# Optimization experiments

Measured on AMD Instinct MI355X. Metric: run time of the kernel, lower is better.

## Reference

```python
import jax, jax.numpy as jnp
import numpy as np

BS, N, DX, DE, DY, NH = 4, 256, 256, 64, 64, 8
DF = DX // NH


def setup_inputs() -> dict:
    key = jax.random.key(0)
    ks = jax.random.split(key, 24)

    def w(k, i, o):
        return jax.random.normal(k, (i, o), jnp.float32) / jnp.sqrt(jnp.float32(i))

    d = {}
    d["x"] = jax.random.normal(ks[0], (BS, N, DX), jnp.float32)
    d["e"] = jax.random.normal(ks[1], (BS, N, N, DE), jnp.float32)
    d["y"] = jax.random.normal(ks[2], (BS, DY), jnp.float32)
    d["node_mask"] = jnp.ones((BS, N), jnp.float32)
    # projections (use_bias=False in the module)
    d["Wq"] = w(ks[3], DX, DX)
    d["Wk"] = w(ks[4], DX, DX)
    d["Wv"] = w(ks[5], DX, DX)
    d["We_mul"] = w(ks[6], DE, DX)
    d["We_add"] = w(ks[7], DE, DX)
    d["Wye_add"] = w(ks[8], DY, DX)
    d["Wye_mul"] = w(ks[9], DY, DX)
    d["Wyx_add"] = w(ks[10], DY, DX)
    d["Wyx_mul"] = w(ks[11], DY, DX)
    d["Wyy"] = w(ks[12], DY, DY)
    # pooled-feature -> y maps (Xtoy / Etoy use 4*d features: mean,min,max,std)
    d["Wxy"] = w(ks[13], 4 * DX, DY)
    d["bxy"] = jnp.zeros((DY,), jnp.float32)
    d["Wey"] = w(ks[14], 4 * DE, DY)
    d["bey"] = jnp.zeros((DY,), jnp.float32)
    # output heads (bias=True, flax Dense default)
    d["We_out"] = w(ks[15], DX, DE)
    d["be_out"] = jnp.zeros((DE,), jnp.float32)
    d["Wx_out"] = w(ks[16], DX, DX)
    d["bx_out"] = jnp.zeros((DX,), jnp.float32)
    d["Wy_out"] = w(ks[17], DY, DY)
    d["by_out"] = jnp.zeros((DY,), jnp.float32)
    return d


def reference(x, e, y, node_mask, Wq, Wk, Wv, We_mul, We_add, Wye_add, Wye_mul,
              Wyx_add, Wyx_mul, Wyy, Wxy, bxy, Wey, bey, We_out, be_out,
              Wx_out, bx_out, Wy_out, by_out):
    bs, n, dx = x.shape
    nh, df = NH, DF
    x_mask = node_mask[..., None]                       # (bs,n,1)
    e_mask1 = x_mask[:, :, None, :]                     # (bs,n,1,1)
    e_mask2 = x_mask[:, None, :, :]                     # (bs,1,n,1)
    em = e_mask1 * e_mask2                              # (bs,n,n,1)

    q = (x @ Wq) * x_mask
    k = (x @ Wk) * x_mask
    Q = q.reshape(bs, n, 1, nh, df)                     # (bs,n,1,h,df)
    K = k.reshape(bs, 1, n, nh, df)                     # (bs,1,n,h,df)
    Y = Q * K / jnp.sqrt(jnp.float32(df))               # (bs,n,n,h,df) per-channel scores

    e1 = ((e @ We_mul) * em).reshape(bs, n, n, nh, df)
    e2 = ((e @ We_add) * em).reshape(bs, n, n, nh, df)
    Y = Y * (e1 + 1.0) + e2                             # FiLM by edges

    newE = Y.reshape(bs, n, n, dx)
    ye1 = (y @ Wye_add)[:, None, None, :]
    ye2 = (y @ Wye_mul)[:, None, None, :]
    newE = ye1 + (ye2 + 1.0) * newE                     # FiLM by global y
    newE = (newE @ We_out + be_out) * em                # (bs,n,n,de)

    # masked softmax over key axis (axis=2); mask broadcasts over df
    mask5 = e_mask2[..., None] > 0                      # (bs,1,n,1,1)
    attn = jax.nn.softmax(jnp.where(mask5, Y, -1e9), axis=2)

    v = ((x @ Wv) * x_mask).reshape(bs, 1, n, nh, df)
    weighted = (attn * v).sum(axis=2).reshape(bs, n, dx)

    yx1 = (y @ Wyx_add)[:, None, :]
    yx2 = (y @ Wyx_mul)[:, None, :]
    newX = yx1 + (yx2 + 1.0) * weighted
    newX = (newX @ Wx_out + bx_out) * x_mask            # (bs,n,dx)

    def pool(t, axes):
        return jnp.concatenate([t.mean(axis=axes), t.min(axis=axes),
                                t.max(axis=axes), t.std(axis=axes, ddof=1)], axis=-1)

    x_y = pool(x, (1,)) @ Wxy + bxy                     # (bs,dy)
    e_y = pool(e, (1, 2)) @ Wey + bey                   # (bs,dy)
    y_y = y @ Wyy
    newY = (y_y + e_y + x_y) @ Wy_out + by_out          # (bs,dy)
    return newX, newE, newY
```

## Files before the change

### kernel.cpp

```cpp
#include <hip/hip_runtime.h>
#include <hip/hip_bf16.h>

#define BSZ 4
#define NN  256
#define DXX 256
#define DEE 64
#define DYY 64

#define OFF_Q     0
#define OFF_K     262144
#define OFF_V     524288
#define OFF_XW    786432
#define OFF_YE1   1048576
#define OFF_YE2   1049600
#define OFF_YX1   1050624
#define OFF_YX2   1051648
#define OFF_PX    1052672
#define OFF_EPART 1057792

typedef __attribute__((ext_vector_type(8))) short bf16x8;
typedef __attribute__((ext_vector_type(4))) float f32x4;

__device__ __forceinline__ short f2bf(float f) {
    unsigned u = __float_as_uint(f);
    unsigned r = u + 0x7fffu + ((u >> 16) & 1u);
    return (short)(r >> 16);
}

__device__ __forceinline__ unsigned cvt_pk_bf16(float lo, float hi) {
    unsigned r;
    asm("v_cvt_pk_bf16_f32 %0, %1, %2" : "=v"(r) : "v"(lo), "v"(hi));
    return r;
}

__device__ __forceinline__ void pack8_store(const float4& A, const float4& B, short* dst) {
    uint4 v;
    v.x = cvt_pk_bf16(A.x, A.y);
    v.y = cvt_pk_bf16(A.z, A.w);
    v.z = cvt_pk_bf16(B.x, B.y);
    v.w = cvt_pk_bf16(B.z, B.w);
    *(uint4*)dst = v;
}

__global__ __launch_bounds__(256) void prep_kernel(
    const float* __restrict__ x, const float* __restrict__ e, const float* __restrict__ y,
    const float* __restrict__ nm,
    const float* __restrict__ Wq, const float* __restrict__ Wk, const float* __restrict__ Wv,
    const float* __restrict__ Wye_add, const float* __restrict__ Wye_mul,
    const float* __restrict__ Wyx_add, const float* __restrict__ Wyx_mul,
    float* __restrict__ ws) {

    __shared__ float smem[16 * 256];
    const int blk = blockIdx.x;
    const int t = threadIdx.x;

    if (blk < 192) {
        const int m0 = (blk & 63) * 16;
        const int which = blk >> 6;
        const float* W = which == 0 ? Wq : (which == 1 ? Wk : Wv);
        float* out = ws + (size_t)which * 262144;
        float (*xl)[256] = (float(*)[256])smem;
        for (int r = 0; r < 16; ++r) xl[r][t] = x[(m0 + r) * 256 + t];
        __syncthreads();
        float acc[16];
#pragma unroll
        for (int r = 0; r < 16; ++r) acc[r] = 0.f;
        for (int d = 0; d < 256; d += 4) {
            float w0 = W[(d + 0) * 256 + t];
            float w1 = W[(d + 1) * 256 + t];
            float w2 = W[(d + 2) * 256 + t];
            float w3 = W[(d + 3) * 256 + t];
#pragma unroll
            for (int r = 0; r < 16; ++r) {
                float4 ev = *(const float4*)&xl[r][d];
                acc[r] = fmaf(ev.x, w0, fmaf(ev.y, w1, fmaf(ev.z, w2, fmaf(ev.w, w3, acc[r]))));
            }
        }
#pragma unroll
        for (int r = 0; r < 16; ++r) {
            int m = m0 + r;
            out[m * 256 + t] = acc[r] * nm[m];
        }
    } else if (blk < 196) {
        const int b = blk - 192;
        float a1 = 0.f, a2 = 0.f, a3 = 0.f, a4 = 0.f;
        for (int k = 0; k < DYY; ++k) {
            float yv = y[b * DYY + k];
            a1 = fmaf(yv, Wye_add[k * 256 + t], a1);
            a2 = fmaf(yv, Wye_mul[k * 256 + t], a2);
            a3 = fmaf(yv, Wyx_add[k * 256 + t], a3);
            a4 = fmaf(yv, Wyx_mul[k * 256 + t], a4);
        }
        ws[OFF_YE1 + b * 256 + t] = a1;
        ws[OFF_YE2 + b * 256 + t] = a2;
        ws[OFF_YX1 + b * 256 + t] = a3;
        ws[OFF_YX2 + b * 256 + t] = a4;
    } else if (blk < 452) {
        const int idx = blk - 196;
        const int s = idx & 63, bb = idx >> 6;
        const int dq = (t & 15) * 4, g = t >> 4;
        const float* base = e + ((size_t)bb * 65536 + s * 1024) * 64;
        float s0 = 0.f, s1 = 0.f, s2 = 0.f, s3 = 0.f;
        float q0 = 0.f, q1 = 0.f, q2 = 0.f, q3 = 0.f;
        float mn0 = 1e30f, mn1 = 1e30f, mn2 = 1e30f, mn3 = 1e30f;
        float mx0 = -1e30f, mx1 = -1e30f, mx2 = -1e30f, mx3 = -1e30f;
#pragma unroll 4
        for (int rr = 0; rr < 64; ++rr) {
            const int row = g * 64 + rr;
            float4 v = *(const float4*)&base[row * 64 + dq];
            s0 += v.x; s1 += v.y; s2 += v.z; s3 += v.w;
            q0 = fmaf(v.x, v.x, q0); q1 = fmaf(v.y, v.y, q1);
            q2 = fmaf(v.z, v.z, q2); q3 = fmaf(v.w, v.w, q3);
            mn0 = fminf(mn0, v.x); mn1 = fminf(mn1, v.y);
            mn2 = fminf(mn2, v.z); mn3 = fminf(mn3, v.w);
            mx0 = fmaxf(mx0, v.x); mx1 = fmaxf(mx1, v.y);
            mx2 = fmaxf(mx2, v.z); mx3 = fmaxf(mx3, v.w);
        }
        float (*red)[16][64] = (float(*)[16][64])smem;
        red[0][g][dq + 0] = s0;  red[0][g][dq + 1] = s1;  red[0][g][dq + 2] = s2;  red[0][g][dq + 3] = s3;
        red[1][g][dq + 0] = q0;  red[1][g][dq + 1] = q1;  red[1][g][dq + 2] = q2;  red[1][g][dq + 3] = q3;
        red[2][g][dq + 0] = mn0; red[2][g][dq + 1] = mn1; red[2][g][dq + 2] = mn2; red[2][g][dq + 3] = mn3;
        red[3][g][dq + 0] = mx0; red[3][g][dq + 1] = mx1; red[3][g][dq + 2] = mx2; red[3][g][dq + 3] = mx3;
        __syncthreads();
        const int stat = t >> 6, d = t & 63;
        float a;
        if (stat < 2) {
            a = 0.f;
            for (int gg = 0; gg < 16; ++gg) a += red[stat][gg][d];
        } else if (stat == 2) {
            a = 1e30f;
            for (int gg = 0; gg < 16; ++gg) a = fminf(a, red[2][gg][d]);
        } else {
            a = -1e30f;
            for (int gg = 0; gg < 16; ++gg) a = fmaxf(a, red[3][gg][d]);
        }
        ws[OFF_EPART + (size_t)((bb * 64 + s) * 64 + d) * 4 + stat] = a;
    } else {
        const int b = blk - 452;
        float s = 0.f, q = 0.f, mn = 1e30f, mx = -1e30f;
        for (int i = 0; i < 256; ++i) {
            float v = x[(b * 256 + i) * 256 + t];
            s += v; q = fmaf(v, v, q);
            mn = fminf(mn, v); mx = fmaxf(mx, v);
        }
        float mean = s * (1.f / 256.f);
        float var  = (q - s * s * (1.f / 256.f)) * (1.f / 255.f);
        var = fmaxf(var, 0.f);
        ws[OFF_PX + b * 1024 + t]       = mean;
        ws[OFF_PX + b * 1024 + 256 + t] = mn;
        ws[OFF_PX + b * 1024 + 512 + t] = mx;
        ws[OFF_PX + b * 1024 + 768 + t] = sqrtf(var);
    }
}

#define EBP  72
#define YPLP 264
#define OBP  68

__global__ __launch_bounds__(256, 2) void fusedmfma_kernel(
    const float* __restrict__ e, const float* __restrict__ nmask,
    const float* __restrict__ Wm, const float* __restrict__ Wa,
    const float* __restrict__ We_out, const float* __restrict__ be_out,
    const float* __restrict__ ws, float* __restrict__ outE, float* __restrict__ xw) {

    const int i = blockIdx.x, b = blockIdx.y;
    const int tid  = threadIdx.x;
    const int w    = tid >> 6;
    const int lane = tid & 63;
    const int quad = lane >> 4, l16 = lane & 15;

    __shared__ __align__(16) short ebuf[2][32 * EBP];
    __shared__ __align__(16) short ypl[2][32 * YPLP];
    __shared__ __align__(16) float obuf[2][32 * OBP];
    __shared__ float nml[256];

    nml[tid] = nmask[b * 256 + tid];

    bf16x8 bm[4][2], ba[4][2], bw[8];
    const int cw = w * 64;
#pragma unroll
    for (int ct = 0; ct < 4; ++ct) {
        const int c = cw + ct * 16 + l16;
#pragma unroll
        for (int s = 0; s < 2; ++s) {
            bf16x8 t1, t2;
#pragma unroll
            for (int jj = 0; jj < 8; ++jj) {
                const int d = s * 32 + quad * 8 + jj;
                t1[jj] = f2bf(Wm[d * 256 + c]);
                t2[jj] = f2bf(Wa[d * 256 + c]);
            }
            bm[ct][s] = t1; ba[ct][s] = t2;
        }
    }
    const int cp = w * 16 + l16;
    {
#pragma unroll
        for (int s = 0; s < 8; ++s) {
            bf16x8 t;
#pragma unroll
            for (int jj = 0; jj < 8; ++jj) {
                const int cch = s * 32 + quad * 8 + jj;
                t[jj] = f2bf(We_out[cch * 64 + cp]);
            }
            bw[s] = t;
        }
    }
    const float bo = be_out[cp];

    const float rs = 0.17677669529663687f;
    float qc[4], ye1c[4], ye2c[4];
#pragma unroll
    for (int ct = 0; ct < 4; ++ct) {
        const int c = cw + ct * 16 + l16;
        qc[ct]   = ws[OFF_Q + (size_t)(b * 256 + i) * 256 + c] * rs;
        ye1c[ct] = ws[OFF_YE1 + b * 256 + c];
        ye2c[ct] = ws[OFF_YE2 + b * 256 + c] + 1.f;
    }
    const float* kb = ws + OFF_K + (size_t)b * 65536;
    const float* vb = ws + OFF_V + (size_t)b * 65536;

    const float* eb = e + ((size_t)(b * 256 + i)) * 256 * 64;
    const int jr = tid >> 3, c0 = (tid & 7) * 8;
    {
        float4 A = *(const float4*)(eb + jr * 64 + c0);
        float4 B = *(const float4*)(eb + jr * 64 + c0 + 4);
        pack8_store(A, B, &ebuf[0][jr * EBP + c0]);
    }
    __syncthreads();
    const float mi = nml[i];
    const size_t outbase = (size_t)(b * 256 + i) * 256;

    float msm[4], lsm[4], wsm[4];
#pragma unroll
    for (int ct = 0; ct < 4; ++ct) { msm[ct] = -1e30f; lsm[ct] = 0.f; wsm[ct] = 0.f; }

    for (int chunk = 0; chunk < 8; ++chunk) {
        const int cur = chunk & 1, j0 = chunk * 32;

        bf16x8 ae[2][2];
#pragma unroll
        for (int jt = 0; jt < 2; ++jt)
#pragma unroll
            for (int s = 0; s < 2; ++s)
                ae[jt][s] = *(const bf16x8*)&ebuf[cur][(jt * 16 + l16) * EBP + s * 32 + quad * 8];

        float4 pfA, pfB;
        if (chunk < 7) {
            const float* nb = eb + (size_t)(j0 + 32 + jr) * 64 + c0;
            pfA = *(const float4*)(nb);
            pfB = *(const float4*)(nb + 4);
        }

        float emv[8];
#pragma unroll
        for (int jt = 0; jt < 2; ++jt)
#pragma unroll
            for (int r = 0; r < 4; ++r)
                emv[jt * 4 + r] = mi * nml[j0 + jt * 16 + quad * 4 + r];

        for (int ct = 0; ct < 4; ++ct) {
            const int c = cw + ct * 16 + l16;
            float Ks[8], Vs[8];
#pragma unroll
            for (int jt = 0; jt < 2; ++jt)
#pragma unroll
                for (int r = 0; r < 4; ++r) {
                    const int jg = j0 + jt * 16 + quad * 4 + r;
                    Ks[jt * 4 + r] = kb[jg * 256 + c];
                    Vs[jt * 4 + r] = vb[jg * 256 + c];
                }

            f32x4 a1_0 = {0.f, 0.f, 0.f, 0.f}, a1_1 = {0.f, 0.f, 0.f, 0.f};
            f32x4 a2_0 = {0.f, 0.f, 0.f, 0.f}, a2_1 = {0.f, 0.f, 0.f, 0.f};
#pragma unroll
            for (int s = 0; s < 2; ++s) {
                a1_0 = __builtin_amdgcn_mfma_f32_16x16x32_bf16(ae[0][s], bm[ct][s], a1_0, 0, 0, 0);
                a1_1 = __builtin_amdgcn_mfma_f32_16x16x32_bf16(ae[1][s], bm[ct][s], a1_1, 0, 0, 0);
                a2_0 = __builtin_amdgcn_mfma_f32_16x16x32_bf16(ae[0][s], ba[ct][s], a2_0, 0, 0, 0);
                a2_1 = __builtin_amdgcn_mfma_f32_16x16x32_bf16(ae[1][s], ba[ct][s], a2_1, 0, 0, 0);
            }

            float Ys[8];
#pragma unroll
            for (int jt = 0; jt < 2; ++jt) {
                float yv[4];
#pragma unroll
                for (int r = 0; r < 4; ++r) {
                    const int u  = jt * 4 + r;
                    const float e1v = (jt == 0) ? a1_0[r] : a1_1[r];
                    const float e2v = (jt == 0) ? a2_0[r] : a2_1[r];
                    const float em = emv[u];
                    const float Yv = fmaf(qc[ct] * Ks[u], fmaf(e1v, em, 1.f), e2v * em);
                    yv[r] = fmaf(ye2c[ct], Yv, ye1c[ct]);
                    Ys[u] = (em > 0.f) ? Yv : -1e9f;
                }
                const int jl0 = jt * 16 + quad * 4;
                unsigned short* yb = (unsigned short*)&ypl[cur][jl0 * YPLP + c];
                const unsigned p01 = cvt_pk_bf16(yv[0], yv[1]);
                const unsigned p23 = cvt_pk_bf16(yv[2], yv[3]);
                yb[0]        = (unsigned short)p01;
                yb[YPLP]     = (unsigned short)(p01 >> 16);
                yb[2 * YPLP] = (unsigned short)p23;
                yb[3 * YPLP] = (unsigned short)(p23 >> 16);
            }
            float cm = Ys[0];
#pragma unroll
            for (int u = 1; u < 8; ++u) cm = fmaxf(cm, Ys[u]);
            const float mnew = fmaxf(msm[ct], cm);
            const float al = __expf(msm[ct] - mnew);
            float sum = 0.f, wsum = 0.f;
#pragma unroll
            for (int u = 0; u < 8; ++u) {
                const float p = __expf(Ys[u] - mnew);
                sum += p; wsum = fmaf(p, Vs[u], wsum);
            }
            lsm[ct] = fmaf(lsm[ct], al, sum);
            wsm[ct] = fmaf(wsm[ct], al, wsum);
            msm[ct] = mnew;
        }

        if (chunk < 7) pack8_store(pfA, pfB, &ebuf[cur ^ 1][jr * EBP + c0]);
        __syncthreads();

        f32x4 acc0 = {0.f, 0.f, 0.f, 0.f}, acc1 = {0.f, 0.f, 0.f, 0.f};
#pragma unroll
        for (int s = 0; s < 8; ++s) {
            bf16x8 a0 = *(const bf16x8*)&ypl[cur][(l16) * YPLP + s * 32 + quad * 8];
            bf16x8 a1 = *(const bf16x8*)&ypl[cur][(16 + l16) * YPLP + s * 32 + quad * 8];
            acc0 = __builtin_amdgcn_mfma_f32_16x16x32_bf16(a0, bw[s], acc0, 0, 0, 0);
            acc1 = __builtin_amdgcn_mfma_f32_16x16x32_bf16(a1, bw[s], acc1, 0, 0, 0);
        }
#pragma unroll
        for (int jt = 0; jt < 2; ++jt)
#pragma unroll
            for (int r = 0; r < 4; ++r) {
                const int jl = jt * 16 + quad * 4 + r;
                const float em2 = mi * nml[j0 + jl];
                const float av = (jt == 0) ? acc0[r] : acc1[r];
                obuf[cur][jl * OBP + cp] = (av + bo) * em2;
            }
        if (chunk > 0) {
            const int pj0 = j0 - 32;
            const float4 A  = *(const float4*)&obuf[cur ^ 1][jr * OBP + c0];
            const float4 Bv = *(const float4*)&obuf[cur ^ 1][jr * OBP + c0 + 4];
            float* dst = outE + (outbase + pj0 + jr) * 64 + c0;
            *(float4*)dst = A; *(float4*)(dst + 4) = Bv;
        }
    }
    __syncthreads();
    {
        const float4 A  = *(const float4*)&obuf[1][jr * OBP + c0];
        const float4 Bv = *(const float4*)&obuf[1][jr * OBP + c0 + 4];
        float* dst = outE + (outbase + 224 + jr) * 64 + c0;
        *(float4*)dst = A; *(float4*)(dst + 4) = Bv;
    }

#pragma unroll
    for (int ct = 0; ct < 4; ++ct) {
        float m = msm[ct], l = lsm[ct], wv = wsm[ct];
#pragma unroll
        for (int off = 16; off < 64; off <<= 1) {
            const float m2 = __shfl_xor(m, off, 64);
            const float l2 = __shfl_xor(l, off, 64);
            const float w2 = __shfl_xor(wv, off, 64);
            const float mn = fmaxf(m, m2);
            const float s1 = __expf(m - mn), s2 = __expf(m2 - mn);
            l = l * s1 + l2 * s2;
            wv = wv * s1 + w2 * s2;
            m = mn;
        }
        if (quad == 0) {
            const int c = cw + ct * 16 + l16;
            const float weighted = wv / l;
            const float yx1 = ws[OFF_YX1 + b * 256 + c];
            const float yx2 = ws[OFF_YX2 + b * 256 + c] + 1.f;
            xw[(size_t)(b * 256 + i) * 256 + c] = fmaf(yx2, weighted, yx1);
        }
    }
}

__global__ __launch_bounds__(256) void post_kernel(
    const float* __restrict__ xwin, const float* __restrict__ Wx_out,
    const float* __restrict__ bx_out, const float* __restrict__ nm,
    const float* __restrict__ y,
    const float* __restrict__ Wyy, const float* __restrict__ Wxy,
    const float* __restrict__ bxy, const float* __restrict__ Wey,
    const float* __restrict__ bey, const float* __restrict__ Wy_out,
    const float* __restrict__ by_out,
    const float* __restrict__ ws, float* __restrict__ outX, float* __restrict__ outY) {

    __shared__ float smem[16 * 256];
    const int blk = blockIdx.x;
    const int t = threadIdx.x;

    if (blk < 64) {
        const int m0 = blk * 16;
        float (*xl)[256] = (float(*)[256])smem;
        for (int r = 0; r < 16; ++r) xl[r][t] = xwin[(m0 + r) * 256 + t];
        __syncthreads();
        float acc[16];
#pragma unroll
        for (int r = 0; r < 16; ++r) acc[r] = 0.f;
        for (int d = 0; d < 256; d += 4) {
            float w0 = Wx_out[(d + 0) * 256 + t];
            float w1 = Wx_out[(d + 1) * 256 + t];
            float w2 = Wx_out[(d + 2) * 256 + t];
            float w3 = Wx_out[(d + 3) * 256 + t];
#pragma unroll
            for (int r = 0; r < 16; ++r) {
                float4 ev = *(const float4*)&xl[r][d];
                acc[r] = fmaf(ev.x, w0, fmaf(ev.y, w1, fmaf(ev.z, w2, fmaf(ev.w, w3, acc[r]))));
            }
        }
        const float bv = bx_out[t];
#pragma unroll
        for (int r = 0; r < 16; ++r) {
            int m = m0 + r;
            outX[m * 256 + t] = (acc[r] + bv) * nm[m];
        }
    } else {
        const int b = blk - 64;
        const int d = t & 63, g = t >> 6;
        {
            float S = 0.f, Q = 0.f, Mn = 1e30f, Mx = -1e30f;
            for (int ss = g * 16; ss < g * 16 + 16; ++ss) {
                const float* ep = ws + OFF_EPART + ((b * 64 + ss) * 64 + d) * 4;
                float4 p = *(const float4*)ep;
                S += p.x; Q += p.y; Mn = fminf(Mn, p.z); Mx = fmaxf(Mx, p.w);
            }
            float (*red)[4][64] = (float(*)[4][64])smem;
            red[0][g][d] = S; red[1][g][d] = Q; red[2][g][d] = Mn; red[3][g][d] = Mx;
        }
        __syncthreads();
        float* pe = smem + 1024;
        if (g == 0) {
            float (*red)[4][64] = (float(*)[4][64])smem;
            float S = 0.f, Q = 0.f, Mn = 1e30f, Mx = -1e30f;
#pragma unroll
            for (int gg = 0; gg < 4; ++gg) {
                S += red[0][gg][d]; Q += red[1][gg][d];
                Mn = fminf(Mn, red[2][gg][d]); Mx = fmaxf(Mx, red[3][gg][d]);
            }
            const float n = 65536.f;
            float meane = S / n;
            float vare  = (Q - S * S / n) / (n - 1.f);
            vare = fmaxf(vare, 0.f);
            pe[d]       = meane;
            pe[64 + d]  = Mn;
            pe[128 + d] = Mx;
            pe[192 + d] = sqrtf(vare);
        }
        __syncthreads();
        const int o = t & 63, ks = t >> 6;
        float a = 0.f;
        if (ks == 0) {
            a = bxy[o] + bey[o];
            for (int k = 0; k < 64; ++k) a = fmaf(y[b * 64 + k], Wyy[k * 64 + o], a);
        }
        for (int k = ks * 64; k < ks * 64 + 64; ++k) a = fmaf(pe[k], Wey[k * 64 + o], a);
        const float* px = ws + OFF_PX + b * 1024;
        for (int k = ks * 256; k < ks * 256 + 256; ++k) a = fmaf(px[k], Wxy[k * 64 + o], a);
        float* redB = smem + 1280;
        redB[ks * 64 + o] = a;
        __syncthreads();
        float* sy = smem + 1536;
        if (ks == 0) sy[o] = redB[o] + redB[64 + o] + redB[128 + o] + redB[192 + o];
        __syncthreads();
        if (t < 64) {
            float r = by_out[t];
            for (int k = 0; k < 64; ++k) r = fmaf(sy[k], Wy_out[k * 64 + t], r);
            outY[b * 64 + t] = r;
        }
    }
}

extern "C" void kernel_launch(void* const* d_in, const int* in_sizes, int n_in,
                              void* d_out, int out_size, void* d_ws, size_t ws_size,
                              hipStream_t stream) {
    const float* x        = (const float*)d_in[0];
    const float* e        = (const float*)d_in[1];
    const float* y        = (const float*)d_in[2];
    const float* nm       = (const float*)d_in[3];
    const float* Wq       = (const float*)d_in[4];
    const float* Wk       = (const float*)d_in[5];
    const float* Wv       = (const float*)d_in[6];
    const float* We_mul   = (const float*)d_in[7];
    const float* We_add   = (const float*)d_in[8];
    const float* Wye_add  = (const float*)d_in[9];
    const float* Wye_mul  = (const float*)d_in[10];
    const float* Wyx_add  = (const float*)d_in[11];
    const float* Wyx_mul  = (const float*)d_in[12];
    const float* Wyy      = (const float*)d_in[13];
    const float* Wxy      = (const float*)d_in[14];
    const float* bxy      = (const float*)d_in[15];
    const float* Wey      = (const float*)d_in[16];
    const float* bey      = (const float*)d_in[17];
    const float* We_out   = (const float*)d_in[18];
    const float* be_out   = (const float*)d_in[19];
    const float* Wx_out   = (const float*)d_in[20];
    const float* bx_out   = (const float*)d_in[21];
    const float* Wy_out   = (const float*)d_in[22];
    const float* by_out   = (const float*)d_in[23];

    float* ws   = (float*)d_ws;
    float* outX = (float*)d_out;
    float* outE = (float*)d_out + 262144;
    float* outY = (float*)d_out + 262144 + 16777216;

    prep_kernel<<<456, 256, 0, stream>>>(x, e, y, nm, Wq, Wk, Wv,
                                         Wye_add, Wye_mul, Wyx_add, Wyx_mul, ws);
    fusedmfma_kernel<<<dim3(256, 4), 256, 0, stream>>>(e, nm, We_mul, We_add, We_out, be_out,
                                                       ws, outE, ws + OFF_XW);
    post_kernel<<<68, 256, 0, stream>>>(ws + OFF_XW, Wx_out, bx_out, nm, y,
                                        Wyy, Wxy, bxy, Wey, bey, Wy_out, by_out,
                                        ws, outX, outY);
}
```

Before: 332.9 us.

## Store edge outputs directly with nontemporal stores and prefetch K/V per column tile

Removes the double-buffered obuf LDS staging for the edge output and writes each MFMA result straight to global memory with nontemporal scalar stores. The Y-plane buffer becomes single-buffered, with a trailing barrier added each chunk. K/V loads for the next column tile are software-prefetched into registers before the current tile's MFMAs. Together these cut LDS use to raise occupancy and hide global load latency. The cost is less coalesced scattered 4-byte output writes, an extra barrier per chunk, and higher register pressure.

```diff
diff --git a/kernel.cpp b/kernel.cpp
--- a/kernel.cpp
+++ b/kernel.cpp
@@ -155,7 +155,6 @@
 
 #define EBP  72
 #define YPLP 264
-#define OBP  68
 
 __global__ __launch_bounds__(256, 2) void fusedmfma_kernel(
     const float* __restrict__ e, const float* __restrict__ nmask,
@@ -170,8 +169,7 @@
     const int quad = lane >> 4, l16 = lane & 15;
 
     __shared__ __align__(16) short ebuf[2][32 * EBP];
-    __shared__ __align__(16) short ypl[2][32 * YPLP];
-    __shared__ __align__(16) float obuf[2][32 * OBP];
+    __shared__ __align__(16) short ypl[32 * YPLP];
     __shared__ float nml[256];
 
     nml[tid] = nmask[b * 256 + tid];
@@ -238,13 +236,6 @@
     for (int chunk = 0; chunk < 8; ++chunk) {
         const int cur = chunk & 1, j0 = chunk * 32;
 
-        bf16x8 ae[2][2];
-#pragma unroll
-        for (int jt = 0; jt < 2; ++jt)
-#pragma unroll
-            for (int s = 0; s < 2; ++s)
-                ae[jt][s] = *(const bf16x8*)&ebuf[cur][(jt * 16 + l16) * EBP + s * 32 + quad * 8];
-
         float4 pfA, pfB;
         if (chunk < 7) {
             const float* nb = eb + (size_t)(j0 + 32 + jr) * 64 + c0;
@@ -252,6 +243,21 @@
             pfB = *(const float4*)(nb + 4);
         }
 
+        float Ks[8], Vs[8];
+#pragma unroll
+        for (int u = 0; u < 8; ++u) {
+            const int jg = j0 + (u >> 2) * 16 + quad * 4 + (u & 3);
+            Ks[u] = kb[jg * 256 + cw + l16];
+            Vs[u] = vb[jg * 256 + cw + l16];
+        }
+
+        bf16x8 ae[2][2];
+#pragma unroll
+        for (int jt = 0; jt < 2; ++jt)
+#pragma unroll
+            for (int s = 0; s < 2; ++s)
+                ae[jt][s] = *(const bf16x8*)&ebuf[cur][(jt * 16 + l16) * EBP + s * 32 + quad * 8];
+
         float emv[8];
 #pragma unroll
         for (int jt = 0; jt < 2; ++jt)
@@ -259,17 +265,19 @@
             for (int r = 0; r < 4; ++r)
                 emv[jt * 4 + r] = mi * nml[j0 + jt * 16 + quad * 4 + r];
 
+#pragma unroll 4
         for (int ct = 0; ct < 4; ++ct) {
             const int c = cw + ct * 16 + l16;
-            float Ks[8], Vs[8];
-#pragma unroll
-            for (int jt = 0; jt < 2; ++jt)
-#pragma unroll
-                for (int r = 0; r < 4; ++r) {
-                    const int jg = j0 + jt * 16 + quad * 4 + r;
-                    Ks[jt * 4 + r] = kb[jg * 256 + c];
-                    Vs[jt * 4 + r] = vb[jg * 256 + c];
+
+            float Kn[8], Vn[8];
+            if (ct < 3) {
+#pragma unroll
+                for (int u = 0; u < 8; ++u) {
+                    const int jg = j0 + (u >> 2) * 16 + quad * 4 + (u & 3);
+                    Kn[u] = kb[jg * 256 + c + 16];
+                    Vn[u] = vb[jg * 256 + c + 16];
                 }
+            }
 
             f32x4 a1_0 = {0.f, 0.f, 0.f, 0.f}, a1_1 = {0.f, 0.f, 0.f, 0.f};
             f32x4 a2_0 = {0.f, 0.f, 0.f, 0.f}, a2_1 = {0.f, 0.f, 0.f, 0.f};
@@ -296,7 +304,7 @@
                     Ys[u] = (em > 0.f) ? Yv : -1e9f;
                 }
                 const int jl0 = jt * 16 + quad * 4;
-                unsigned short* yb = (unsigned short*)&ypl[cur][jl0 * YPLP + c];
+                unsigned short* yb = (unsigned short*)&ypl[jl0 * YPLP + c];
                 const unsigned p01 = cvt_pk_bf16(yv[0], yv[1]);
                 const unsigned p23 = cvt_pk_bf16(yv[2], yv[3]);
                 yb[0]        = (unsigned short)p01;
@@ -318,6 +326,11 @@
             lsm[ct] = fmaf(lsm[ct], al, sum);
             wsm[ct] = fmaf(wsm[ct], al, wsum);
             msm[ct] = mnew;
+
+            if (ct < 3) {
+#pragma unroll
+                for (int u = 0; u < 8; ++u) { Ks[u] = Kn[u]; Vs[u] = Vn[u]; }
+            }
         }
 
         if (chunk < 7) pack8_store(pfA, pfB, &ebuf[cur ^ 1][jr * EBP + c0]);
@@ -326,8 +339,8 @@
         f32x4 acc0 = {0.f, 0.f, 0.f, 0.f}, acc1 = {0.f, 0.f, 0.f, 0.f};
 #pragma unroll
         for (int s = 0; s < 8; ++s) {
-            bf16x8 a0 = *(const bf16x8*)&ypl[cur][(l16) * YPLP + s * 32 + quad * 8];
-            bf16x8 a1 = *(const bf16x8*)&ypl[cur][(16 + l16) * YPLP + s * 32 + quad * 8];
+            bf16x8 a0 = *(const bf16x8*)&ypl[(l16) * YPLP + s * 32 + quad * 8];
+            bf16x8 a1 = *(const bf16x8*)&ypl[(16 + l16) * YPLP + s * 32 + quad * 8];
             acc0 = __builtin_amdgcn_mfma_f32_16x16x32_bf16(a0, bw[s], acc0, 0, 0, 0);
             acc1 = __builtin_amdgcn_mfma_f32_16x16x32_bf16(a1, bw[s], acc1, 0, 0, 0);
         }
@@ -336,24 +349,13 @@
 #pragma unroll
             for (int r = 0; r < 4; ++r) {
                 const int jl = jt * 16 + quad * 4 + r;
-                const float em2 = mi * nml[j0 + jl];
+                const int jg = j0 + jl;
+                const float em2 = mi * nml[jg];
                 const float av = (jt == 0) ? acc0[r] : acc1[r];
-                obuf[cur][jl * OBP + cp] = (av + bo) * em2;
-            }
-        if (chunk > 0) {
-            const int pj0 = j0 - 32;
-            const float4 A  = *(const float4*)&obuf[cur ^ 1][jr * OBP + c0];
-            const float4 Bv = *(const float4*)&obuf[cur ^ 1][jr * OBP + c0 + 4];
-            float* dst = outE + (outbase + pj0 + jr) * 64 + c0;
-            *(float4*)dst = A; *(float4*)(dst + 4) = Bv;
-        }
-    }
-    __syncthreads();
-    {
-        const float4 A  = *(const float4*)&obuf[1][jr * OBP + c0];
-        const float4 Bv = *(const float4*)&obuf[1][jr * OBP + c0 + 4];
-        float* dst = outE + (outbase + 224 + jr) * 64 + c0;
-        *(float4*)dst = A; *(float4*)(dst + 4) = Bv;
+                __builtin_nontemporal_store((av + bo) * em2,
+                                            &outE[(outbase + jg) * 64 + cp]);
+            }
+        __syncthreads();
     }
 
 #pragma unroll
```

Result: faster. 309.5 us (-7.0%).

## Store K/V transposed for vector loads and write edge output directly

Applied to the files above, without the earlier changes.

The projection stage now writes K and V transposed (channel-major per batch), so the fused kernel can fetch eight key positions per channel with two float4 loads instead of eight strided scalar loads. The LDS staging buffer for the edge output is removed and results are stored straight to global memory from the MFMA accumulators. The edge-tile LDS reads move after the prefetch issue, and the channel-tile loop is unrolled. The direct stores write one float per lane with a 64-float stride across rows, which may coalesce worse than the old float4 rows. The transposed K/V writes in the projection kernel are also strided.

```diff
diff --git a/kernel.cpp b/kernel.cpp
--- a/kernel.cpp
+++ b/kernel.cpp
@@ -76,10 +76,23 @@
                 acc[r] = fmaf(ev.x, w0, fmaf(ev.y, w1, fmaf(ev.z, w2, fmaf(ev.w, w3, acc[r]))));
             }
         }
-#pragma unroll
-        for (int r = 0; r < 16; ++r) {
-            int m = m0 + r;
-            out[m * 256 + t] = acc[r] * nm[m];
+        if (which == 0) {
+#pragma unroll
+            for (int r = 0; r < 16; ++r) {
+                int m = m0 + r;
+                out[m * 256 + t] = acc[r] * nm[m];
+            }
+        } else {
+            const int bb2  = m0 >> 8;
+            const int jloc = m0 & 255;
+            float tv[16];
+#pragma unroll
+            for (int r = 0; r < 16; ++r) tv[r] = acc[r] * nm[m0 + r];
+            float* outb = out + (size_t)bb2 * 65536 + t * 256 + jloc;
+#pragma unroll
+            for (int g = 0; g < 4; ++g)
+                *(float4*)&outb[g * 4] =
+                    make_float4(tv[4 * g], tv[4 * g + 1], tv[4 * g + 2], tv[4 * g + 3]);
         }
     } else if (blk < 196) {
         const int b = blk - 192;
@@ -155,7 +168,6 @@
 
 #define EBP  72
 #define YPLP 264
-#define OBP  68
 
 __global__ __launch_bounds__(256, 2) void fusedmfma_kernel(
     const float* __restrict__ e, const float* __restrict__ nmask,
@@ -171,7 +183,6 @@
 
     __shared__ __align__(16) short ebuf[2][32 * EBP];
     __shared__ __align__(16) short ypl[2][32 * YPLP];
-    __shared__ __align__(16) float obuf[2][32 * OBP];
     __shared__ float nml[256];
 
     nml[tid] = nmask[b * 256 + tid];
@@ -217,8 +228,8 @@
         ye1c[ct] = ws[OFF_YE1 + b * 256 + c];
         ye2c[ct] = ws[OFF_YE2 + b * 256 + c] + 1.f;
     }
-    const float* kb = ws + OFF_K + (size_t)b * 65536;
-    const float* vb = ws + OFF_V + (size_t)b * 65536;
+    const float* kTb = ws + OFF_K + (size_t)b * 65536;
+    const float* vTb = ws + OFF_V + (size_t)b * 65536;
 
     const float* eb = e + ((size_t)(b * 256 + i)) * 256 * 64;
     const int jr = tid >> 3, c0 = (tid & 7) * 8;
@@ -238,13 +249,6 @@
     for (int chunk = 0; chunk < 8; ++chunk) {
         const int cur = chunk & 1, j0 = chunk * 32;
 
-        bf16x8 ae[2][2];
-#pragma unroll
-        for (int jt = 0; jt < 2; ++jt)
-#pragma unroll
-            for (int s = 0; s < 2; ++s)
-                ae[jt][s] = *(const bf16x8*)&ebuf[cur][(jt * 16 + l16) * EBP + s * 32 + quad * 8];
-
         float4 pfA, pfB;
         if (chunk < 7) {
             const float* nb = eb + (size_t)(j0 + 32 + jr) * 64 + c0;
@@ -252,6 +256,13 @@
             pfB = *(const float4*)(nb + 4);
         }
 
+        bf16x8 ae[2][2];
+#pragma unroll
+        for (int jt = 0; jt < 2; ++jt)
+#pragma unroll
+            for (int s = 0; s < 2; ++s)
+                ae[jt][s] = *(const bf16x8*)&ebuf[cur][(jt * 16 + l16) * EBP + s * 32 + quad * 8];
+
         float emv[8];
 #pragma unroll
         for (int jt = 0; jt < 2; ++jt)
@@ -259,17 +270,16 @@
             for (int r = 0; r < 4; ++r)
                 emv[jt * 4 + r] = mi * nml[j0 + jt * 16 + quad * 4 + r];
 
+#pragma unroll
         for (int ct = 0; ct < 4; ++ct) {
             const int c = cw + ct * 16 + l16;
-            float Ks[8], Vs[8];
-#pragma unroll
-            for (int jt = 0; jt < 2; ++jt)
-#pragma unroll
-                for (int r = 0; r < 4; ++r) {
-                    const int jg = j0 + jt * 16 + quad * 4 + r;
-                    Ks[jt * 4 + r] = kb[jg * 256 + c];
-                    Vs[jt * 4 + r] = vb[jg * 256 + c];
-                }
+
+            const float4 K0 = *(const float4*)&kTb[c * 256 + j0 + quad * 4];
+            const float4 K1 = *(const float4*)&kTb[c * 256 + j0 + 16 + quad * 4];
+            const float4 V0 = *(const float4*)&vTb[c * 256 + j0 + quad * 4];
+            const float4 V1 = *(const float4*)&vTb[c * 256 + j0 + 16 + quad * 4];
+            const float Ks[8] = {K0.x, K0.y, K0.z, K0.w, K1.x, K1.y, K1.z, K1.w};
+            const float Vs[8] = {V0.x, V0.y, V0.z, V0.w, V1.x, V1.y, V1.z, V1.w};
 
             f32x4 a1_0 = {0.f, 0.f, 0.f, 0.f}, a1_1 = {0.f, 0.f, 0.f, 0.f};
             f32x4 a2_0 = {0.f, 0.f, 0.f, 0.f}, a2_1 = {0.f, 0.f, 0.f, 0.f};
@@ -336,24 +346,11 @@
 #pragma unroll
             for (int r = 0; r < 4; ++r) {
                 const int jl = jt * 16 + quad * 4 + r;
-                const float em2 = mi * nml[j0 + jl];
+                const int jg = j0 + jl;
+                const float em2 = mi * nml[jg];
                 const float av = (jt == 0) ? acc0[r] : acc1[r];
-                obuf[cur][jl * OBP + cp] = (av + bo) * em2;
-            }
-        if (chunk > 0) {
-            const int pj0 = j0 - 32;
-            const float4 A  = *(const float4*)&obuf[cur ^ 1][jr * OBP + c0];
-            const float4 Bv = *(const float4*)&obuf[cur ^ 1][jr * OBP + c0 + 4];
-            float* dst = outE + (outbase + pj0 + jr) * 64 + c0;
-            *(float4*)dst = A; *(float4*)(dst + 4) = Bv;
-        }
-    }
-    __syncthreads();
-    {
-        const float4 A  = *(const float4*)&obuf[1][jr * OBP + c0];
-        const float4 Bv = *(const float4*)&obuf[1][jr * OBP + c0 + 4];
-        float* dst = outE + (outbase + 224 + jr) * 64 + c0;
-        *(float4*)dst = A; *(float4*)(dst + 4) = Bv;
+                outE[(outbase + jg) * 64 + cp] = (av + bo) * em2;
+            }
     }
 
 #pragma unroll
```

After: 288.9 us. -13.2%, faster.
